# Performance work log

Hardware: AMD Instinct MI355X
Metric: run time of the kernel (lower is better)

The kernel has to match this reference:

```python
import jax, jax.numpy as jnp
import numpy as np

NUM_HEADS = 8
NUM_GROUPS = 8
NUM_ITERATIONS = 3
DT = 0.1
EPS = 1e-5


def group_norm(x, scale, bias):
    # x: [B, C, H, W], GroupNorm(8, C)
    B, C, H, W = x.shape
    xg = x.reshape(B, NUM_GROUPS, C // NUM_GROUPS, H, W)
    mean = xg.mean(axis=(2, 3, 4), keepdims=True)
    var = xg.var(axis=(2, 3, 4), keepdims=True)
    xg = (xg - mean) * jax.lax.rsqrt(var + EPS)
    x = xg.reshape(B, C, H, W)
    return x * scale[None, :, None, None] + bias[None, :, None, None]


def setup_inputs() -> dict:
    key = jax.random.key(0)
    ks = jax.random.split(key, 4)
    B, C, H, W = 8, 512, 32, 32
    x = jax.random.normal(ks[0], (B, C, H, W), dtype=jnp.float32)
    qkv_w = jax.random.normal(ks[1], (3 * C, C), dtype=jnp.float32) * (1.0 / np.sqrt(C))
    proj_w = jax.random.normal(ks[2], (C, C), dtype=jnp.float32) * (1.0 / np.sqrt(C))
    inl_w = jax.random.normal(ks[3], (C, C), dtype=jnp.float32) * (1.0 / np.sqrt(C))
    return {
        "x": x,
        "gn_scale": jnp.ones((C,), jnp.float32),
        "gn_bias": jnp.zeros((C,), jnp.float32),
        "qkv_w": qkv_w,
        "qkv_b": jnp.zeros((3 * C,), jnp.float32),
        "proj_w": proj_w,
        "proj_b": jnp.zeros((C,), jnp.float32),
        "inl_w": inl_w,
        "inl_b": jnp.zeros((C,), jnp.float32),
    }


def reference(x, gn_scale, gn_bias, qkv_w, qkv_b, proj_w, proj_b, inl_w, inl_b):
    B, C, H, W = x.shape
    nh = NUM_HEADS
    hd = C // nh
    S = H * W

    h = group_norm(x, gn_scale, gn_bias)

    # 1x1 conv == channel matmul
    qkv = jnp.einsum('oc,bchw->bohw', qkv_w, h) + qkv_b[None, :, None, None]
    q, k, v = jnp.split(qkv, 3, axis=1)  # each [B, C, H, W]

    def to_heads(t):  # [B, C, H, W] -> [B, nh, S, hd]
        return t.reshape(B, nh, hd, S).transpose(0, 1, 3, 2)

    q, k, v = to_heads(q), to_heads(k), to_heads(v)

    scale = hd ** (-0.5)
    attn = jax.nn.softmax(jnp.einsum('bnsd,bntd->bnst', q, k) * scale, axis=-1)
    h = jnp.einsum('bnst,bntd->bnsd', attn, v)  # [B, nh, S, hd]

    # back to [B, S, C] for INL refinement
    h_flat = h.transpose(0, 1, 3, 2).reshape(B, C, S).transpose(0, 2, 1)

    # SimpleINLDynamics: iterative Euler refinement x <- x + dt * tanh(W x + b)
    def step(hf, _):
        hf = hf + DT * jnp.tanh(jnp.einsum('bsc,oc->bso', hf, inl_w) + inl_b)
        return hf, None
    h_flat, _ = jax.lax.scan(step, h_flat, None, length=NUM_ITERATIONS)

    h = h_flat.transpose(0, 2, 1).reshape(B, C, H, W)
    h = jnp.einsum('oc,bchw->bohw', proj_w, h) + proj_b[None, :, None, None]
    return x + h
```

## Files before the change

kernel.cpp:

```cpp
#include <hip/hip_runtime.h>
#include <math.h>

#define B_ 8
#define C_ 512
#define S_ 1024
#define HD 64
#define NHEADS 8
#define NGROUPS 8
#define DT_STEP 0.1f
#define EPS_GN 1e-5f
#define LOG2E 1.4426950408889634f

typedef __attribute__((ext_vector_type(8))) short bf16x8;
typedef __attribute__((ext_vector_type(4))) float f32x4;
typedef __attribute__((ext_vector_type(8))) unsigned short ushort8;
typedef __attribute__((ext_vector_type(4))) unsigned short ushort4_t;

static __device__ __forceinline__ unsigned short f2bf(float f) {
  unsigned int u = __builtin_bit_cast(unsigned int, f);
  u += 0x7fff + ((u >> 16) & 1);
  return (unsigned short)(u >> 16);
}

static __device__ __forceinline__ unsigned short f2bf_fast(float f) {
  unsigned int u = __builtin_bit_cast(unsigned int, f);
  return (unsigned short)((u + 0x8000u) >> 16);
}

static __device__ __forceinline__ float bf2f(unsigned short u) {
  unsigned int t = ((unsigned int)u) << 16;
  return __builtin_bit_cast(float, t);
}

static __device__ __forceinline__ float fast_tanh(float x) {
  float xc = fminf(fmaxf(x, -15.f), 15.f);
  float e = exp2f(xc * (2.0f * LOG2E));
  return (e - 1.f) / (e + 1.f);
}

static __device__ __forceinline__ void load16_lds(const void* g, void* l) {
  __builtin_amdgcn_global_load_lds((const __attribute__((address_space(1))) void*)g,
                                   (__attribute__((address_space(3))) void*)l, 16, 0, 0);
}

__global__ __launch_bounds__(256) void prep_kernel(
    const float* __restrict__ a, const float* __restrict__ b, const float* __restrict__ c,
    unsigned short* __restrict__ A, unsigned short* __restrict__ B, unsigned short* __restrict__ C,
    const float* __restrict__ x, float* __restrict__ gpart) {
  int bid = blockIdx.x;
  int tid = threadIdx.x;
  if (bid < 640) {
    const float* src; unsigned short* dst; int off;
    if (bid < 384) { src = a; dst = A; off = bid * 2048; }
    else if (bid < 512) { src = b; dst = B; off = (bid - 384) * 2048; }
    else { src = c; dst = C; off = (bid - 512) * 2048; }
    int i = off + tid * 8;
    f32x4 v0 = *(const f32x4*)(src + i);
    f32x4 v1 = *(const f32x4*)(src + i + 4);
    ushort8 o;
    o[0] = f2bf(v0[0]); o[1] = f2bf(v0[1]); o[2] = f2bf(v0[2]); o[3] = f2bf(v0[3]);
    o[4] = f2bf(v1[0]); o[5] = f2bf(v1[1]); o[6] = f2bf(v1[2]); o[7] = f2bf(v1[3]);
    *(ushort8*)(dst + i) = o;
    return;
  }
  int sbid = bid - 640;
  int bg = sbid >> 3, chunk = sbid & 7;
  const float* xp = x + (size_t)bg * 65536 + (size_t)chunk * 8192;
  float sum = 0.f, sq = 0.f;
  #pragma unroll
  for (int i = 0; i < 8; ++i) {
    f32x4 v = *(const f32x4*)(xp + i * 1024 + tid * 4);
    sum += v[0] + v[1] + v[2] + v[3];
    sq += v[0]*v[0] + v[1]*v[1] + v[2]*v[2] + v[3]*v[3];
  }
  #pragma unroll
  for (int off = 32; off >= 1; off >>= 1) {
    sum += __shfl_xor(sum, off, 64);
    sq  += __shfl_xor(sq, off, 64);
  }
  __shared__ float s1[4], s2[4];
  int wave = tid >> 6, lane = tid & 63;
  if (lane == 0) { s1[wave] = sum; s2[wave] = sq; }
  __syncthreads();
  if (tid == 0) {
    float S = s1[0] + s1[1] + s1[2] + s1[3];
    float Q = s2[0] + s2[1] + s2[2] + s2[3];
    gpart[bg * 16 + chunk * 2] = S;
    gpart[bg * 16 + chunk * 2 + 1] = Q;
  }
}

__global__ __launch_bounds__(256) void gn_apply_t(
    const float* __restrict__ x, const float* __restrict__ gpart,
    const float* __restrict__ scale, const float* __restrict__ bias,
    unsigned short* __restrict__ h_t) {
  int bid = blockIdx.x;
  int bg = bid >> 4, st = bid & 15;
  int b = bg >> 3, g = bg & 7;
  float S = 0.f, Q = 0.f;
  #pragma unroll
  for (int i = 0; i < 8; ++i) {
    S += gpart[bg * 16 + i * 2];
    Q += gpart[bg * 16 + i * 2 + 1];
  }
  float mean = S / 65536.f;
  float var = Q / 65536.f - mean * mean;
  float inv = rsqrtf(var + EPS_GN);

  int tid = threadIdx.x;
  int sl = tid >> 2;
  int cq = (tid & 3) * 16;
  float sA[16], sB[16];
  #pragma unroll
  for (int u = 0; u < 16; ++u) {
    float scv = scale[g * 64 + cq + u];
    sA[u] = inv * scv;
    sB[u] = bias[g * 64 + cq + u] - mean * inv * scv;
  }

  const float* xp = x + ((size_t)b * C_ + (size_t)g * 64) * S_;
  __shared__ float tile[64][65];
  #pragma unroll
  for (int it = 0; it < 16; ++it) {
    int lin = it * 256 + tid;
    int c = lin >> 6, s = lin & 63;
    tile[c][s] = xp[(size_t)c * S_ + st * 64 + s];
  }
  __syncthreads();
  unsigned short vals[16];
  #pragma unroll
  for (int u = 0; u < 16; ++u)
    vals[u] = f2bf_fast(tile[cq + u][sl] * sA[u] + sB[u]);
  unsigned short* dst = h_t + ((size_t)b * S_ + st * 64 + sl) * C_ + g * 64 + cq;
  ushort8 lo, hi;
  #pragma unroll
  for (int u = 0; u < 8; ++u) { lo[u] = vals[u]; hi[u] = vals[u + 8]; }
  *(ushort8*)dst = lo;
  *(ushort8*)(dst + 8) = hi;
}

template<int MB, int NB, int WMG, int WNG>
__device__ __forceinline__ void gemm_nt_core(
    const unsigned short* __restrict__ Ab,
    const unsigned short* __restrict__ Bb,
    unsigned short* ldsA, unsigned short* ldsB,
    f32x4* acc) {
  constexpr int TI = (MB / WMG) / 16;
  constexpr int TJ = (NB / WNG) / 16;
  constexpr int NQA = MB * 4 / 256;
  constexpr int NQB = NB * 4 / 256;
  const int K = 512;
  const int tid = threadIdx.x;
  const int w = tid >> 6, lane = tid & 63, quad = lane >> 4, l15 = lane & 15;
  const int wm = (WNG == 1) ? w : ((WMG == 1) ? 0 : (w >> 1));
  const int wn = (WNG == 1) ? 0 : ((WMG == 1) ? w : (w & 1));

  for (int k0 = 0; k0 < K; k0 += 32) {
    __syncthreads();
    #pragma unroll
    for (int q = 0; q < NQA; ++q) {
      int c = q * 256 + tid;
      load16_lds(Ab + (size_t)(c >> 2) * K + k0 + (c & 3) * 8, ldsA + c * 8);
    }
    #pragma unroll
    for (int q = 0; q < NQB; ++q) {
      int c = q * 256 + tid;
      load16_lds(Bb + (size_t)(c >> 2) * K + k0 + (c & 3) * 8, ldsB + c * 8);
    }
    __syncthreads();
    bf16x8 af[TI], bfr[TJ];
    #pragma unroll
    for (int i = 0; i < TI; ++i)
      af[i] = *(const bf16x8*)(ldsA + (wm * (MB / WMG) + i * 16 + l15) * 32 + quad * 8);
    #pragma unroll
    for (int j = 0; j < TJ; ++j)
      bfr[j] = *(const bf16x8*)(ldsB + (wn * (NB / WNG) + j * 16 + l15) * 32 + quad * 8);
    #pragma unroll
    for (int i = 0; i < TI; ++i)
      #pragma unroll
      for (int j = 0; j < TJ; ++j)
        acc[i * TJ + j] = __builtin_amdgcn_mfma_f32_16x16x32_bf16(af[i], bfr[j], acc[i * TJ + j], 0, 0, 0);
  }
}

__global__ __launch_bounds__(256) void gemm_qkv_mfma(
    const unsigned short* __restrict__ Wbf, const unsigned short* __restrict__ h_t,
    const float* __restrict__ bias,
    unsigned short* __restrict__ Qt, unsigned short* __restrict__ Kt,
    unsigned short* __restrict__ Vt) {
  __shared__ __align__(16) unsigned short ldsA[128 * 32];
  __shared__ __align__(16) unsigned short ldsB[128 * 32];
  int b = blockIdx.z;
  int bm = blockIdx.y * 128, bn = blockIdx.x * 128;
  f32x4 acc[16];
  #pragma unroll
  for (int t = 0; t < 16; ++t) acc[t] = (f32x4){0.f, 0.f, 0.f, 0.f};
  gemm_nt_core<128, 128, 2, 2>(Wbf + (size_t)bm * 512,
                               h_t + ((size_t)b * S_ + bn) * 512, ldsA, ldsB, acc);
  int tid = threadIdx.x, w = tid >> 6, lane = tid & 63, quad = lane >> 4, l15 = lane & 15;
  int wm = w >> 1, wn = w & 1;
  int tensor = bm >> 9;
  float qscale = (tensor == 0) ? 0.125f * LOG2E : 1.0f;
  #pragma unroll
  for (int i = 0; i < 4; ++i) {
    #pragma unroll
    for (int j = 0; j < 4; ++j) {
      int m0 = bm + wm * 64 + i * 16 + quad * 4;
      int ng = bn + wn * 64 + j * 16 + l15;
      f32x4 v = acc[i * 4 + j];
      if (tensor < 2) {
        int head = (m0 >> 6) & 7, d0 = m0 & 63;
        ushort4_t pk;
        #pragma unroll
        for (int r = 0; r < 4; ++r) pk[r] = f2bf((v[r] + bias[m0 + r]) * qscale);
        unsigned short* dst = (tensor ? Kt : Qt) +
            (((size_t)(b * 8 + head) * S_ + ng) * 64 + d0);
        *(ushort4_t*)dst = pk;
      } else {
        #pragma unroll
        for (int r = 0; r < 4; ++r)
          Vt[(size_t)b * (C_ * S_) + (size_t)(m0 - 1024 + r) * S_ + ng] = f2bf(v[r] + bias[m0 + r]);
      }
    }
  }
}

__global__ __launch_bounds__(256) void attn_mfma(
    const unsigned short* __restrict__ Qt,
    const unsigned short* __restrict__ Kt,
    const unsigned short* __restrict__ Vt,
    unsigned short* __restrict__ hflat_bf) {
  int tid = threadIdx.x, wave = tid >> 6, lane = tid & 63;
  int quad = lane >> 4, l15 = lane & 15;
  int bid = blockIdx.x;
  int bn = bid & 63, sblk = bid >> 6, b = bn >> 3, n = bn & 7;
  int s0w = sblk * 64 + wave * 16;

  __shared__ unsigned short k_lds[64][72];
  __shared__ unsigned short v_lds[64][72];
  __shared__ unsigned short p_lds[4][16][72];

  const unsigned short* Qb = Qt + (((size_t)(b * 8 + n)) * S_ + s0w + l15) * 64;
  const unsigned short* Kb = Kt + ((size_t)(b * 8 + n)) * S_ * 64;
  const unsigned short* Vb = Vt + ((size_t)b * C_ + n * 64) * S_;

  bf16x8 qa0 = *(const bf16x8*)(Qb + quad * 8);
  bf16x8 qa1 = *(const bf16x8*)(Qb + 32 + quad * 8);

  bf16x8 ones;
  #pragma unroll
  for (int j = 0; j < 8; ++j) ones[j] = (short)0x3F80;

  f32x4 o_acc[4];
  f32x4 l_acc = {0.f, 0.f, 0.f, 0.f};
  #pragma unroll
  for (int dc = 0; dc < 4; ++dc) o_acc[dc] = (f32x4){0.f, 0.f, 0.f, 0.f};

  for (int t0 = 0; t0 < S_; t0 += 64) {
    __syncthreads();
    #pragma unroll
    for (int it = 0; it < 2; ++it) {
      int idx = tid + it * 256;
      int row = idx >> 3, c8 = (idx & 7) * 8;
      *(ushort8*)&k_lds[row][c8] = *(const ushort8*)(Kb + (size_t)(t0 + row) * 64 + c8);
      *(ushort8*)&v_lds[row][c8] = *(const ushort8*)(Vb + (size_t)row * S_ + t0 + c8);
    }
    __syncthreads();

    f32x4 sc[4];
    #pragma unroll
    for (int tc = 0; tc < 4; ++tc) {
      bf16x8 kb0 = *(const bf16x8*)&k_lds[tc * 16 + l15][quad * 8];
      bf16x8 kb1 = *(const bf16x8*)&k_lds[tc * 16 + l15][32 + quad * 8];
      f32x4 c = {0.f, 0.f, 0.f, 0.f};
      c = __builtin_amdgcn_mfma_f32_16x16x32_bf16(qa0, kb0, c, 0, 0, 0);
      sc[tc] = __builtin_amdgcn_mfma_f32_16x16x32_bf16(qa1, kb1, c, 0, 0, 0);
    }

    #pragma unroll
    for (int tc = 0; tc < 4; ++tc)
      #pragma unroll
      for (int r = 0; r < 4; ++r)
        p_lds[wave][quad * 4 + r][tc * 16 + l15] = f2bf_fast(exp2f(sc[tc][r]));

    bf16x8 pa0 = *(const bf16x8*)&p_lds[wave][l15][quad * 8];
    bf16x8 pa1 = *(const bf16x8*)&p_lds[wave][l15][32 + quad * 8];
    l_acc = __builtin_amdgcn_mfma_f32_16x16x32_bf16(pa0, ones, l_acc, 0, 0, 0);
    l_acc = __builtin_amdgcn_mfma_f32_16x16x32_bf16(pa1, ones, l_acc, 0, 0, 0);
    #pragma unroll
    for (int dc = 0; dc < 4; ++dc) {
      bf16x8 vb0 = *(const bf16x8*)&v_lds[dc * 16 + l15][quad * 8];
      bf16x8 vb1 = *(const bf16x8*)&v_lds[dc * 16 + l15][32 + quad * 8];
      o_acc[dc] = __builtin_amdgcn_mfma_f32_16x16x32_bf16(pa0, vb0, o_acc[dc], 0, 0, 0);
      o_acc[dc] = __builtin_amdgcn_mfma_f32_16x16x32_bf16(pa1, vb1, o_acc[dc], 0, 0, 0);
    }
  }

  float inv_l[4];
  #pragma unroll
  for (int r = 0; r < 4; ++r) inv_l[r] = 1.f / l_acc[r];
  #pragma unroll
  for (int dc = 0; dc < 4; ++dc) {
    #pragma unroll
    for (int r = 0; r < 4; ++r) {
      int s = s0w + quad * 4 + r;
      size_t idx = ((size_t)b * S_ + s) * C_ + n * 64 + dc * 16 + l15;
      hflat_bf[idx] = f2bf_fast(o_acc[dc][r] * inv_l[r]);
    }
  }
}

__global__ __launch_bounds__(256) void inl_step_mfma(
    const unsigned short* __restrict__ hbf_in, const unsigned short* __restrict__ Wbf,
    const float* __restrict__ bias, unsigned short* __restrict__ hbf_out) {
  __shared__ __align__(16) unsigned short ldsA[64 * 32];
  __shared__ __align__(16) unsigned short ldsB[128 * 32];
  int bm = blockIdx.y * 64, bn = blockIdx.x * 128;
  f32x4 acc[8];
  #pragma unroll
  for (int t = 0; t < 8; ++t) acc[t] = (f32x4){0.f, 0.f, 0.f, 0.f};
  gemm_nt_core<64, 128, 1, 4>(hbf_in + (size_t)bm * 512,
                              Wbf + (size_t)bn * 512, ldsA, ldsB, acc);
  int tid = threadIdx.x, w = tid >> 6, lane = tid & 63, quad = lane >> 4, l15 = lane & 15;
  #pragma unroll
  for (int i = 0; i < 4; ++i) {
    #pragma unroll
    for (int j = 0; j < 2; ++j) {
      int m0 = bm + i * 16 + quad * 4;
      int o = bn + w * 32 + j * 16 + l15;
      float bv = bias[o];
      f32x4 v = acc[i * 2 + j];
      #pragma unroll
      for (int r = 0; r < 4; ++r) {
        size_t idx = (size_t)(m0 + r) * 512 + o;
        float hin = bf2f(hbf_in[idx]);
        hbf_out[idx] = f2bf_fast(hin + DT_STEP * fast_tanh(v[r] + bv));
      }
    }
  }
}

__global__ __launch_bounds__(256) void gemm_proj_mfma(
    const unsigned short* __restrict__ Wbf, const unsigned short* __restrict__ hbf,
    const float* __restrict__ pb, const float* __restrict__ x,
    float* __restrict__ Out) {
  __shared__ __align__(16) unsigned short ldsA[64 * 32];
  __shared__ __align__(16) unsigned short ldsB[128 * 32];
  int bm = blockIdx.y * 64, bn = blockIdx.x * 128;
  f32x4 acc[8];
  #pragma unroll
  for (int t = 0; t < 8; ++t) acc[t] = (f32x4){0.f, 0.f, 0.f, 0.f};
  gemm_nt_core<64, 128, 1, 4>(Wbf + (size_t)bm * 512,
                              hbf + (size_t)bn * 512, ldsA, ldsB, acc);
  int tid = threadIdx.x, w = tid >> 6, lane = tid & 63, quad = lane >> 4, l15 = lane & 15;
  #pragma unroll
  for (int i = 0; i < 4; ++i) {
    #pragma unroll
    for (int j = 0; j < 2; ++j) {
      int o0 = bm + i * 16 + quad * 4;
      int ng = bn + w * 32 + j * 16 + l15;
      int b = ng >> 10, s = ng & 1023;
      f32x4 v = acc[i * 2 + j];
      #pragma unroll
      for (int r = 0; r < 4; ++r) {
        size_t idx = ((size_t)b * C_ + o0 + r) * S_ + s;
        Out[idx] = x[idx] + pb[o0 + r] + v[r];
      }
    }
  }
}

extern "C" void kernel_launch(void* const* d_in, const int* in_sizes, int n_in,
                              void* d_out, int out_size, void* d_ws, size_t ws_size,
                              hipStream_t stream) {
  const float* x        = (const float*)d_in[0];
  const float* gn_scale = (const float*)d_in[1];
  const float* gn_bias  = (const float*)d_in[2];
  const float* qkv_w    = (const float*)d_in[3];
  const float* qkv_b    = (const float*)d_in[4];
  const float* proj_w   = (const float*)d_in[5];
  const float* proj_b   = (const float*)d_in[6];
  const float* inl_w    = (const float*)d_in[7];
  const float* inl_b    = (const float*)d_in[8];
  float* out = (float*)d_out;
  float* ws = (float*)d_ws;

  unsigned short* Qt  = (unsigned short*)(ws + 8388608);
  unsigned short* Kt  = (unsigned short*)(ws + 10485760);
  unsigned short* Vt  = (unsigned short*)(ws + 12582912);
  unsigned short* h_t = (unsigned short*)(ws + 14680064);
  unsigned short* Bbf = h_t;
  unsigned short* Abf = (unsigned short*)(ws + 16777216);
  float* gpart = ws + 18874368;
  unsigned short* qkvw_bf  = (unsigned short*)(ws + 18878464);
  unsigned short* inlw_bf  = qkvw_bf + 786432;
  unsigned short* projw_bf = inlw_bf + 262144;

  prep_kernel<<<1152, 256, 0, stream>>>(qkv_w, inl_w, proj_w, qkvw_bf, inlw_bf, projw_bf, x, gpart);
  gn_apply_t<<<1024, 256, 0, stream>>>(x, gpart, gn_scale, gn_bias, h_t);
  gemm_qkv_mfma<<<dim3(8, 12, 8), 256, 0, stream>>>(qkvw_bf, h_t, qkv_b, Qt, Kt, Vt);
  attn_mfma<<<1024, 256, 0, stream>>>(Qt, Kt, Vt, Abf);
  inl_step_mfma<<<dim3(4, 128), 256, 0, stream>>>(Abf, inlw_bf, inl_b, Bbf);
  inl_step_mfma<<<dim3(4, 128), 256, 0, stream>>>(Bbf, inlw_bf, inl_b, Abf);
  inl_step_mfma<<<dim3(4, 128), 256, 0, stream>>>(Abf, inlw_bf, inl_b, Bbf);
  gemm_proj_mfma<<<dim3(64, 8), 256, 0, stream>>>(projw_bf, Bbf, proj_b, x, out);
}
```

Before: 218.2 us.

## Prefetch K/V into registers, use raw exp2, shrink INL/proj GEMM tiles

The attention kernel now loads the next K/V tile into registers while computing on the current one, so global load latency can overlap with the MFMA work. exp2f calls are replaced by the raw hardware exp2 builtin in attention and tanh, which drops the range-handling code around them. The INL step and projection GEMMs move from 64x128 tiles with a 1x4 wave layout to 64x64 tiles with a 2x2 layout, doubling the block count for more parallelism at the cost of less operand reuse per block. The register prefetch raises register pressure in the attention kernel.

Result: no change. 216.0 us (-1.0%).

```diff
diff --git a/kernel.cpp b/kernel.cpp
--- a/kernel.cpp
+++ b/kernel.cpp
@@ -32,9 +32,13 @@
   return __builtin_bit_cast(float, t);
 }
 
+static __device__ __forceinline__ float exp2_raw(float x) {
+  return __builtin_amdgcn_exp2f(x);
+}
+
 static __device__ __forceinline__ float fast_tanh(float x) {
   float xc = fminf(fmaxf(x, -15.f), 15.f);
-  float e = exp2f(xc * (2.0f * LOG2E));
+  float e = exp2_raw(xc * (2.0f * LOG2E));
   return (e - 1.f) / (e + 1.f);
 }
 
@@ -256,16 +260,29 @@
   #pragma unroll
   for (int dc = 0; dc < 4; ++dc) o_acc[dc] = (f32x4){0.f, 0.f, 0.f, 0.f};
 
+  int row0 = tid >> 3, c80 = (tid & 7) * 8;
+  int row1 = (tid + 256) >> 3, c81 = c80;
+
+  ushort8 kreg[2], vreg[2];
+  kreg[0] = *(const ushort8*)(Kb + (size_t)row0 * 64 + c80);
+  kreg[1] = *(const ushort8*)(Kb + (size_t)row1 * 64 + c81);
+  vreg[0] = *(const ushort8*)(Vb + (size_t)row0 * S_ + c80);
+  vreg[1] = *(const ushort8*)(Vb + (size_t)row1 * S_ + c81);
+
   for (int t0 = 0; t0 < S_; t0 += 64) {
     __syncthreads();
-    #pragma unroll
-    for (int it = 0; it < 2; ++it) {
-      int idx = tid + it * 256;
-      int row = idx >> 3, c8 = (idx & 7) * 8;
-      *(ushort8*)&k_lds[row][c8] = *(const ushort8*)(Kb + (size_t)(t0 + row) * 64 + c8);
-      *(ushort8*)&v_lds[row][c8] = *(const ushort8*)(Vb + (size_t)row * S_ + t0 + c8);
-    }
+    *(ushort8*)&k_lds[row0][c80] = kreg[0];
+    *(ushort8*)&k_lds[row1][c81] = kreg[1];
+    *(ushort8*)&v_lds[row0][c80] = vreg[0];
+    *(ushort8*)&v_lds[row1][c81] = vreg[1];
     __syncthreads();
+    if (t0 + 64 < S_) {
+      int t1 = t0 + 64;
+      kreg[0] = *(const ushort8*)(Kb + (size_t)(t1 + row0) * 64 + c80);
+      kreg[1] = *(const ushort8*)(Kb + (size_t)(t1 + row1) * 64 + c81);
+      vreg[0] = *(const ushort8*)(Vb + (size_t)row0 * S_ + t1 + c80);
+      vreg[1] = *(const ushort8*)(Vb + (size_t)row1 * S_ + t1 + c81);
+    }
 
     f32x4 sc[4];
     #pragma unroll
@@ -281,7 +298,7 @@
     for (int tc = 0; tc < 4; ++tc)
       #pragma unroll
       for (int r = 0; r < 4; ++r)
-        p_lds[wave][quad * 4 + r][tc * 16 + l15] = f2bf_fast(exp2f(sc[tc][r]));
+        p_lds[wave][quad * 4 + r][tc * 16 + l15] = f2bf_fast(exp2_raw(sc[tc][r]));
 
     bf16x8 pa0 = *(const bf16x8*)&p_lds[wave][l15][quad * 8];
     bf16x8 pa1 = *(const bf16x8*)&p_lds[wave][l15][32 + quad * 8];
@@ -314,20 +331,21 @@
     const unsigned short* __restrict__ hbf_in, const unsigned short* __restrict__ Wbf,
     const float* __restrict__ bias, unsigned short* __restrict__ hbf_out) {
   __shared__ __align__(16) unsigned short ldsA[64 * 32];
-  __shared__ __align__(16) unsigned short ldsB[128 * 32];
-  int bm = blockIdx.y * 64, bn = blockIdx.x * 128;
-  f32x4 acc[8];
-  #pragma unroll
-  for (int t = 0; t < 8; ++t) acc[t] = (f32x4){0.f, 0.f, 0.f, 0.f};
-  gemm_nt_core<64, 128, 1, 4>(hbf_in + (size_t)bm * 512,
-                              Wbf + (size_t)bn * 512, ldsA, ldsB, acc);
+  __shared__ __align__(16) unsigned short ldsB[64 * 32];
+  int bm = blockIdx.y * 64, bn = blockIdx.x * 64;
+  f32x4 acc[4];
+  #pragma unroll
+  for (int t = 0; t < 4; ++t) acc[t] = (f32x4){0.f, 0.f, 0.f, 0.f};
+  gemm_nt_core<64, 64, 2, 2>(hbf_in + (size_t)bm * 512,
+                             Wbf + (size_t)bn * 512, ldsA, ldsB, acc);
   int tid = threadIdx.x, w = tid >> 6, lane = tid & 63, quad = lane >> 4, l15 = lane & 15;
-  #pragma unroll
-  for (int i = 0; i < 4; ++i) {
+  int wm = w >> 1, wn = w & 1;
+  #pragma unroll
+  for (int i = 0; i < 2; ++i) {
     #pragma unroll
     for (int j = 0; j < 2; ++j) {
-      int m0 = bm + i * 16 + quad * 4;
-      int o = bn + w * 32 + j * 16 + l15;
+      int m0 = bm + wm * 32 + i * 16 + quad * 4;
+      int o = bn + wn * 32 + j * 16 + l15;
       float bv = bias[o];
       f32x4 v = acc[i * 2 + j];
       #pragma unroll
@@ -345,20 +363,21 @@
     const float* __restrict__ pb, const float* __restrict__ x,
     float* __restrict__ Out) {
   __shared__ __align__(16) unsigned short ldsA[64 * 32];
-  __shared__ __align__(16) unsigned short ldsB[128 * 32];
-  int bm = blockIdx.y * 64, bn = blockIdx.x * 128;
-  f32x4 acc[8];
-  #pragma unroll
-  for (int t = 0; t < 8; ++t) acc[t] = (f32x4){0.f, 0.f, 0.f, 0.f};
-  gemm_nt_core<64, 128, 1, 4>(Wbf + (size_t)bm * 512,
-                              hbf + (size_t)bn * 512, ldsA, ldsB, acc);
+  __shared__ __align__(16) unsigned short ldsB[64 * 32];
+  int bm = blockIdx.y * 64, bn = blockIdx.x * 64;
+  f32x4 acc[4];
+  #pragma unroll
+  for (int t = 0; t < 4; ++t) acc[t] = (f32x4){0.f, 0.f, 0.f, 0.f};
+  gemm_nt_core<64, 64, 2, 2>(Wbf + (size_t)bm * 512,
+                             hbf + (size_t)bn * 512, ldsA, ldsB, acc);
   int tid = threadIdx.x, w = tid >> 6, lane = tid & 63, quad = lane >> 4, l15 = lane & 15;
-  #pragma unroll
-  for (int i = 0; i < 4; ++i) {
+  int wm = w >> 1, wn = w & 1;
+  #pragma unroll
+  for (int i = 0; i < 2; ++i) {
     #pragma unroll
     for (int j = 0; j < 2; ++j) {
-      int o0 = bm + i * 16 + quad * 4;
-      int ng = bn + w * 32 + j * 16 + l15;
+      int o0 = bm + wm * 32 + i * 16 + quad * 4;
+      int ng = bn + wn * 32 + j * 16 + l15;
       int b = ng >> 10, s = ng & 1023;
       f32x4 v = acc[i * 2 + j];
       #pragma unroll
@@ -400,8 +419,8 @@
   gn_apply_t<<<1024, 256, 0, stream>>>(x, gpart, gn_scale, gn_bias, h_t);
   gemm_qkv_mfma<<<dim3(8, 12, 8), 256, 0, stream>>>(qkvw_bf, h_t, qkv_b, Qt, Kt, Vt);
   attn_mfma<<<1024, 256, 0, stream>>>(Qt, Kt, Vt, Abf);
-  inl_step_mfma<<<dim3(4, 128), 256, 0, stream>>>(Abf, inlw_bf, inl_b, Bbf);
-  inl_step_mfma<<<dim3(4, 128), 256, 0, stream>>>(Bbf, inlw_bf, inl_b, Abf);
-  inl_step_mfma<<<dim3(4, 128), 256, 0, stream>>>(Abf, inlw_bf, inl_b, Bbf);
-  gemm_proj_mfma<<<dim3(64, 8), 256, 0, stream>>>(projw_bf, Bbf, proj_b, x, out);
-}
+  inl_step_mfma<<<dim3(8, 128), 256, 0, stream>>>(Abf, inlw_bf, inl_b, Bbf);
+  inl_step_mfma<<<dim3(8, 128), 256, 0, stream>>>(Bbf, inlw_bf, inl_b, Abf);
+  inl_step_mfma<<<dim3(8, 128), 256, 0, stream>>>(Abf, inlw_bf, inl_b, Bbf);
+  gemm_proj_mfma<<<dim3(128, 8), 256, 0, stream>>>(projw_bf, Bbf, proj_b, x, out);
+}
```
